# Optimization experiments

Hardware: AMD Instinct MI355X
Metric: run time of the kernel (lower is better)

The kernel has to match this reference:

```python
import jax, jax.numpy as jnp
import numpy as np

B, S, D = 1, 2048, 4096
H, HK, HD = 32, 8, 128  # query heads, kv heads, head dim
T_CACHE = 2048
N_REP = H // HK


def setup_inputs() -> dict:
    key = jax.random.key(0)
    ks = jax.random.split(key, 8)
    x = jax.random.normal(ks[0], (B, S, D), dtype=jnp.float32)
    # multiplicative rope factor, broadcast over head axis
    rope = jax.random.uniform(ks[1], (1, S, 1, HD), dtype=jnp.float32, minval=-1.0, maxval=1.0)
    cache_k = jax.random.normal(ks[2], (B, T_CACHE, HK, HD), dtype=jnp.float32)
    cache_v = jax.random.normal(ks[3], (B, T_CACHE, HK, HD), dtype=jnp.float32)
    wq = jax.random.normal(ks[4], (D, H * HD), dtype=jnp.float32) * 0.02
    wk = jax.random.normal(ks[5], (D, HK * HD), dtype=jnp.float32) * 0.02
    wv = jax.random.normal(ks[6], (D, HK * HD), dtype=jnp.float32) * 0.02
    wo = jax.random.normal(ks[7], (H * HD, D), dtype=jnp.float32) * 0.02
    # mask: [1, 1, S, T_CACHE + S]; attend freely to cache, causal within new chunk
    neg = np.float32(-1e9)
    causal = np.triu(np.full((S, S), neg, dtype=np.float32), k=1)
    mask = np.concatenate([np.zeros((S, T_CACHE), dtype=np.float32), causal], axis=1)
    mask = jnp.asarray(mask)[None, None, :, :]
    return {"x": x, "rope": rope, "mask": mask, "cache_k": cache_k,
            "cache_v": cache_v, "wq": wq, "wk": wk, "wv": wv, "wo": wo}


def reference(x, rope, mask, cache_k, cache_v, wq, wk, wv, wo):
    b, s, _ = x.shape
    scale = 1.0 / np.sqrt(HD).astype(np.float32)
    xq = (x @ wq).reshape(b, s, H, HD) * rope          # [b, s, H, hd]
    xk = (x @ wk).reshape(b, s, HK, HD) * rope         # [b, s, HK, hd]
    xv = (x @ wv).reshape(b, s, HK, HD)
    keys = jnp.concatenate([cache_k, xk], axis=1)      # [b, t, HK, hd]
    vals = jnp.concatenate([cache_v, xv], axis=1)
    keys = jnp.repeat(keys, N_REP, axis=2)             # GQA repeat -> [b, t, H, hd]
    vals = jnp.repeat(vals, N_REP, axis=2)
    scores = jnp.einsum('bshd,bthd->bhst', xq, keys) * scale
    scores = scores + mask
    probs = jax.nn.softmax(scores.astype(jnp.float32), axis=-1).astype(xq.dtype)
    out = jnp.einsum('bhst,bthd->bshd', probs, vals).reshape(b, s, H * HD)
    return out @ wo
```

## Files before the change

### kernel.cpp

```cpp
#include <hip/hip_runtime.h>

typedef unsigned short u16;
typedef unsigned int   u32;
typedef short  s16x8 __attribute__((ext_vector_type(8)));
typedef float  f32x4 __attribute__((ext_vector_type(4)));

__device__ __forceinline__ u16 f2bf(float f) {
    union { float f; u32 i; } x; x.f = f;
    u32 r = x.i + 0x7FFFu + ((x.i >> 16) & 1u);
    return (u16)(r >> 16);
}

__device__ __forceinline__ void gld16(const void* g, void* l) {
    __builtin_amdgcn_global_load_lds((const __attribute__((address_space(1))) void*)g,
                                     (__attribute__((address_space(3))) void*)l,
                                     16, 0, 0);
}

__global__ __launch_bounds__(256)
void cast_bf16(const float* __restrict__ in, u16* __restrict__ out, int n4) {
    int g = blockIdx.x * 256 + threadIdx.x;
    if (g >= n4) return;
    float4 v = ((const float4*)in)[g];
    ushort4 o; o.x = f2bf(v.x); o.y = f2bf(v.y); o.z = f2bf(v.z); o.w = f2bf(v.w);
    ((ushort4*)out)[g] = o;
}

__global__ __launch_bounds__(256)
void tconv(const float* __restrict__ B, u16* __restrict__ Bt, int K, int N) {
    __shared__ float T[32][33];
    int n0 = blockIdx.x * 32, k0 = blockIdx.y * 32;
    int t = threadIdx.x;
    int r = t >> 3, c4 = (t & 7) * 4;
    float4 v = *(const float4*)&B[(size_t)(k0 + r) * N + n0 + c4];
    T[r][c4 + 0] = v.x; T[r][c4 + 1] = v.y; T[r][c4 + 2] = v.z; T[r][c4 + 3] = v.w;
    __syncthreads();
    ushort4 o;
    o.x = f2bf(T[c4 + 0][r]); o.y = f2bf(T[c4 + 1][r]);
    o.z = f2bf(T[c4 + 2][r]); o.w = f2bf(T[c4 + 3][r]);
    *(ushort4*)&Bt[(size_t)(n0 + r) * K + k0 + c4] = o;
}

__global__ __launch_bounds__(256)
void kcache_conv(const float* __restrict__ ck, u16* __restrict__ Kc) {
    int g = blockIdx.x * 256 + threadIdx.x;
    int d = (g & 31) * 4, kh = (g >> 5) & 7, t = g >> 8;
    float4 v = *(const float4*)&ck[(size_t)t * 1024 + kh * 128 + d];
    ushort4 o; o.x = f2bf(v.x); o.y = f2bf(v.y); o.z = f2bf(v.z); o.w = f2bf(v.w);
    *(ushort4*)&Kc[(size_t)kh * 524288 + (size_t)t * 128 + d] = o;
}

__global__ __launch_bounds__(256)
void vcache_conv(const float* __restrict__ cv, u16* __restrict__ Vt) {
    __shared__ float T[32][33];
    int t0 = blockIdx.x * 32, d0 = blockIdx.y * 32, kh = blockIdx.z;
    int t = threadIdx.x;
    int r = t >> 3, c4 = (t & 7) * 4;
    float4 v = *(const float4*)&cv[(size_t)(t0 + r) * 1024 + kh * 128 + d0 + c4];
    T[r][c4 + 0] = v.x; T[r][c4 + 1] = v.y; T[r][c4 + 2] = v.z; T[r][c4 + 3] = v.w;
    __syncthreads();
    ushort4 o;
    o.x = f2bf(T[c4 + 0][r]); o.y = f2bf(T[c4 + 1][r]);
    o.z = f2bf(T[c4 + 2][r]); o.w = f2bf(T[c4 + 3][r]);
    *(ushort4*)&Vt[(size_t)(kh * 128 + d0 + r) * 4096 + t0 + c4] = o;
}

__device__ __forceinline__ void gemm_core(const u16* __restrict__ A,
                                          const u16* __restrict__ Bt,
                                          int K, int m0,
                                          u16* As, u16* Bs, f32x4 acc[4][4])
{
    const int tid = threadIdx.x;
    const int lane = tid & 63, w = tid >> 6;
    const int quad = lane >> 4, l15 = lane & 15;
    const int mw = (w >> 1) * 64, nw = (w & 1) * 64;
    const int lrow = tid >> 2;
    const int lcol = ((tid & 3) ^ (lrow & 3)) * 8;
    const int rsw = l15 & 3;

    for (int k0 = 0; k0 < K; k0 += 32) {
        __syncthreads();
        gld16(A  + (size_t)(m0 +      lrow) * K + k0 + lcol, &As[w * 512]);
        gld16(A  + (size_t)(m0 + 64 + lrow) * K + k0 + lcol, &As[2048 + w * 512]);
        gld16(Bt + (size_t)(           lrow) * K + k0 + lcol, &Bs[w * 512]);
        gld16(Bt + (size_t)(      64 + lrow) * K + k0 + lcol, &Bs[2048 + w * 512]);
        __syncthreads();
        s16x8 af[4], bf[4];
        #pragma unroll
        for (int i = 0; i < 4; ++i)
            af[i] = *(const s16x8*)&As[(mw + i * 16 + l15) * 32 + (quad ^ rsw) * 8];
        #pragma unroll
        for (int j = 0; j < 4; ++j)
            bf[j] = *(const s16x8*)&Bs[(nw + j * 16 + l15) * 32 + (quad ^ rsw) * 8];
        #pragma unroll
        for (int i = 0; i < 4; ++i)
            #pragma unroll
            for (int j = 0; j < 4; ++j)
                acc[i][j] = __builtin_amdgcn_mfma_f32_16x16x32_bf16(
                    af[i], bf[j], acc[i][j], 0, 0, 0);
    }
}

__global__ __launch_bounds__(256, 2)
void gemm_qkv(const u16* __restrict__ A, const u16* __restrict__ Wq,
              const u16* __restrict__ Wk, const u16* __restrict__ Wv,
              u16* __restrict__ Qw, u16* __restrict__ Kc, u16* __restrict__ Vt,
              const float* __restrict__ rope)
{
    __shared__ u16 As[128 * 32];
    __shared__ u16 Bs[128 * 32];
    const int m0 = blockIdx.y * 128, n0 = blockIdx.x * 128;

    const u16* Bt;
    if (n0 < 4096)       Bt = Wq + (size_t)n0 * 4096;
    else if (n0 < 5120)  Bt = Wk + (size_t)(n0 - 4096) * 4096;
    else                 Bt = Wv + (size_t)(n0 - 5120) * 4096;

    f32x4 acc[4][4];
    #pragma unroll
    for (int i = 0; i < 4; ++i)
        #pragma unroll
        for (int j = 0; j < 4; ++j) acc[i][j] = (f32x4)0.f;

    gemm_core(A, Bt, 4096, m0, As, Bs, acc);

    const int lane = threadIdx.x & 63, w = threadIdx.x >> 6;
    const int quad = lane >> 4, l15 = lane & 15;
    const int mw = (w >> 1) * 64, nw = (w & 1) * 64;

    #pragma unroll
    for (int i = 0; i < 4; ++i) {
        #pragma unroll
        for (int j = 0; j < 4; ++j) {
            int mm = m0 + mw + i * 16 + quad * 4;
            int nn = n0 + nw + j * 16 + l15;
            if (nn < 4096) {
                #pragma unroll
                for (int r = 0; r < 4; ++r)
                    Qw[(size_t)(mm + r) * 4096 + nn] =
                        f2bf(acc[i][j][r] * rope[(size_t)(mm + r) * 128 + (nn & 127)]
                             * 0.08838834764831845f);
            } else if (nn < 5120) {
                #pragma unroll
                for (int r = 0; r < 4; ++r)
                    Kc[(size_t)((nn - 4096) >> 7) * 524288
                       + (size_t)(2048 + mm + r) * 128 + (nn & 127)] =
                        f2bf(acc[i][j][r] * rope[(size_t)(mm + r) * 128 + (nn & 127)]);
            } else {
                ushort4 o;
                o.x = f2bf(acc[i][j][0]); o.y = f2bf(acc[i][j][1]);
                o.z = f2bf(acc[i][j][2]); o.w = f2bf(acc[i][j][3]);
                *(ushort4*)&Vt[(size_t)(nn - 5120) * 4096 + 2048 + mm] = o;
            }
        }
    }
}

__global__ __launch_bounds__(256, 2)
void gemm_wo(const u16* __restrict__ A, const u16* __restrict__ Bt,
             float* __restrict__ C)
{
    __shared__ u16 As[128 * 32];
    __shared__ u16 Bs[128 * 32];
    const int m0 = blockIdx.y * 128, n0 = blockIdx.x * 128;

    f32x4 acc[4][4];
    #pragma unroll
    for (int i = 0; i < 4; ++i)
        #pragma unroll
        for (int j = 0; j < 4; ++j) acc[i][j] = (f32x4)0.f;

    gemm_core(A, Bt + (size_t)n0 * 4096, 4096, m0, As, Bs, acc);

    const int lane = threadIdx.x & 63, w = threadIdx.x >> 6;
    const int quad = lane >> 4, l15 = lane & 15;
    const int mw = (w >> 1) * 64, nw = (w & 1) * 64;

    #pragma unroll
    for (int i = 0; i < 4; ++i)
        #pragma unroll
        for (int j = 0; j < 4; ++j) {
            int mm = m0 + mw + i * 16 + quad * 4;
            int nn = n0 + nw + j * 16 + l15;
            #pragma unroll
            for (int r = 0; r < 4; ++r)
                C[(size_t)(mm + r) * 4096 + nn] = acc[i][j][r];
        }
}

__global__ __launch_bounds__(256, 4)
void attn_mfma(const u16* __restrict__ Qw, const u16* __restrict__ Kc,
               const u16* __restrict__ Vt, u16* __restrict__ AO)
{
    __shared__ u16 KsBuf[2][32 * 128];
    __shared__ u16 VsBuf[2][128 * 32];
    __shared__ u16 PbBuf[2][64 * 32];

    const int tid = threadIdx.x;
    const int lane = tid & 63, w = tid >> 6;
    const int quad = lane >> 4, l15 = lane & 15;

    const int bid = blockIdx.x + 32 * blockIdx.y;
    const int kh = bid & 7;
    const int inner = bid >> 3;
    const int h = kh * 4 + (inner & 3);
    const int q0 = (inner >> 2) * 64;

    const int kw = w & 1, qw = w >> 1;
    const size_t kvb = (size_t)kh * 524288;

    s16x8 qreg[2][4];
    #pragma unroll
    for (int n = 0; n < 2; ++n)
        #pragma unroll
        for (int ks = 0; ks < 4; ++ks)
            qreg[n][ks] = *(const s16x8*)&Qw[(size_t)(q0 + qw * 32 + n * 16 + l15) * 4096
                                             + h * 128 + ks * 32 + quad * 8];

    f32x4 o[2][4];
    #pragma unroll
    for (int m = 0; m < 2; ++m)
        #pragma unroll
        for (int n = 0; n < 4; ++n) o[m][n] = (f32x4)0.f;
    float lacc[2] = {0.f, 0.f};

    const int krow = tid >> 4, kcol = ((tid & 15) ^ (krow & 15)) * 8;
    const int vrow = tid >> 2, vcol = ((tid & 3) ^ ((vrow >> 1) & 3)) * 8;

    const u16* kpg = Kc + kvb + (size_t)krow * 128 + kcol;
    const u16* vpg = Vt + kvb + (size_t)vrow * 4096 + vcol;

    const int kend = 2112 + q0;

    u16* ks_rd = &KsBuf[0][0]; u16* ks_st = &KsBuf[1][0];
    u16* vs_rd = &VsBuf[1][0]; u16* vs_st = &VsBuf[0][0];
    u16* pb_wr = &PbBuf[0][0]; u16* pb_rd = &PbBuf[1][0];

    auto PV = [&](const u16* vs, const u16* pb) {
        int vr0 = w * 32 + l15;
        int vr1 = w * 32 + 16 + l15;
        s16x8 vf0 = *(const s16x8*)&vs[vr0 * 32 + (quad ^ ((vr0 >> 1) & 3)) * 8];
        s16x8 vf1 = *(const s16x8*)&vs[vr1 * 32 + (quad ^ ((vr1 >> 1) & 3)) * 8];
        #pragma unroll
        for (int n = 0; n < 4; ++n) {
            int q = n * 16 + l15;
            s16x8 pf = *(const s16x8*)&pb[q * 32 + ((quad ^ (q & 3)) * 8)];
            o[0][n] = __builtin_amdgcn_mfma_f32_16x16x32_bf16(vf0, pf, o[0][n], 0, 0, 0);
            o[1][n] = __builtin_amdgcn_mfma_f32_16x16x32_bf16(vf1, pf, o[1][n], 0, 0, 0);
        }
    };

    gld16(kpg,        &ks_rd[w * 512]);
    gld16(kpg + 2048, &ks_rd[2048 + w * 512]);

    for (int t0 = 0; t0 < kend; t0 += 32) {
        __syncthreads();

        if (t0 + 32 < kend) {
            gld16(kpg + (size_t)(t0 + 32) * 128,        &ks_st[w * 512]);
            gld16(kpg + (size_t)(t0 + 32) * 128 + 2048, &ks_st[2048 + w * 512]);
        }
        gld16(vpg + t0,          &vs_st[w * 512]);
        gld16(vpg + 262144 + t0, &vs_st[2048 + w * 512]);

        f32x4 sc[2];
        sc[0] = (f32x4)0.f; sc[1] = (f32x4)0.f;
        #pragma unroll
        for (int ks = 0; ks < 4; ++ks) {
            int kc8 = (((ks * 4 + quad) ^ l15) & 15) * 8;
            s16x8 kf = *(const s16x8*)&ks_rd[(kw * 16 + l15) * 128 + kc8];
            sc[0] = __builtin_amdgcn_mfma_f32_16x16x32_bf16(kf, qreg[0][ks], sc[0], 0, 0, 0);
            sc[1] = __builtin_amdgcn_mfma_f32_16x16x32_bf16(kf, qreg[1][ks], sc[1], 0, 0, 0);
        }

        const bool maskt = (t0 + 31 > 2048 + q0);
        #pragma unroll
        for (int n2 = 0; n2 < 2; ++n2) {
            float e0 = __expf(sc[n2][0]);
            float e1 = __expf(sc[n2][1]);
            float e2 = __expf(sc[n2][2]);
            float e3 = __expf(sc[n2][3]);
            if (maskt) {
                int key = t0 + kw * 16 + quad * 4;
                int qv  = q0 + qw * 32 + n2 * 16 + l15;
                if (key + 0 >= 2048 && key + 0 - 2048 > qv) e0 = 0.f;
                if (key + 1 >= 2048 && key + 1 - 2048 > qv) e1 = 0.f;
                if (key + 2 >= 2048 && key + 2 - 2048 > qv) e2 = 0.f;
                if (key + 3 >= 2048 && key + 3 - 2048 > qv) e3 = 0.f;
            }
            lacc[n2] += (e0 + e1) + (e2 + e3);
            u32 p0, p1;
            asm("v_cvt_pk_bf16_f32 %0, %1, %2" : "=v"(p0) : "v"(e0), "v"(e1));
            asm("v_cvt_pk_bf16_f32 %0, %1, %2" : "=v"(p1) : "v"(e2), "v"(e3));
            int q = qw * 32 + n2 * 16 + l15;
            uint2 pk; pk.x = p0; pk.y = p1;
            *(uint2*)&pb_wr[q * 32 + (((2 * kw + (quad >> 1)) ^ (q & 3)) * 8)
                            + (quad & 1) * 4] = pk;
        }

        if (t0) PV(vs_rd, pb_rd);

        u16* tp;
        tp = ks_rd; ks_rd = ks_st; ks_st = tp;
        tp = vs_rd; vs_rd = vs_st; vs_st = tp;
        tp = pb_rd; pb_rd = pb_wr; pb_wr = tp;
    }

    __syncthreads();
    PV(vs_rd, pb_rd);

    float* Ls = (float*)&KsBuf[0][0];
    lacc[0] += __shfl_xor(lacc[0], 16); lacc[0] += __shfl_xor(lacc[0], 32);
    lacc[1] += __shfl_xor(lacc[1], 16); lacc[1] += __shfl_xor(lacc[1], 32);
    if (lane < 16) {
        Ls[kw * 64 + qw * 32 +      lane] = lacc[0];
        Ls[kw * 64 + qw * 32 + 16 + lane] = lacc[1];
    }
    __syncthreads();

    #pragma unroll
    for (int n = 0; n < 4; ++n) {
        int qq = n * 16 + l15;
        float inv = 1.f / (Ls[qq] + Ls[64 + qq]);
        #pragma unroll
        for (int m = 0; m < 2; ++m) {
            ushort4 ov;
            ov.x = f2bf(o[m][n][0] * inv);
            ov.y = f2bf(o[m][n][1] * inv);
            ov.z = f2bf(o[m][n][2] * inv);
            ov.w = f2bf(o[m][n][3] * inv);
            *(ushort4*)&AO[(size_t)(q0 + qq) * 4096 + h * 128
                           + w * 32 + m * 16 + quad * 4] = ov;
        }
    }
}

extern "C" void kernel_launch(void* const* d_in, const int* in_sizes, int n_in,
                              void* d_out, int out_size, void* d_ws, size_t ws_size,
                              hipStream_t stream)
{
    const float* x      = (const float*)d_in[0];
    const float* rope   = (const float*)d_in[1];
    const float* cacheK = (const float*)d_in[3];
    const float* cacheV = (const float*)d_in[4];
    const float* wq     = (const float*)d_in[5];
    const float* wk     = (const float*)d_in[6];
    const float* wv     = (const float*)d_in[7];
    const float* wo     = (const float*)d_in[8];
    float* out = (float*)d_out;

    u16* xb = (u16*)d_ws;
    u16* W0 = xb + (size_t)8388608;
    u16* W1 = W0 + (size_t)16777216;
    u16* Qw = W1 + (size_t)4194304;
    u16* Kc = Qw + (size_t)8388608;
    u16* Vt = Kc + (size_t)4194304;
    u16* AO = Vt + (size_t)4194304;
    u16* Wv = AO;

    dim3 blk(256);
    cast_bf16<<<dim3(8192), blk, 0, stream>>>(x, xb, 2097152);
    tconv<<<dim3(128, 128), blk, 0, stream>>>(wq, W0, 4096, 4096);
    tconv<<<dim3(32, 128), blk, 0, stream>>>(wk, W1, 4096, 1024);
    tconv<<<dim3(32, 128), blk, 0, stream>>>(wv, Wv, 4096, 1024);
    gemm_qkv<<<dim3(48, 16), blk, 0, stream>>>(xb, W0, W1, Wv, Qw, Kc, Vt, rope);
    kcache_conv<<<dim3(2048), blk, 0, stream>>>(cacheK, Kc);
    vcache_conv<<<dim3(64, 4, 8), blk, 0, stream>>>(cacheV, Vt);
    attn_mfma<<<dim3(32, 32), blk, 0, stream>>>(Qw, Kc, Vt, AO);
    tconv<<<dim3(128, 128), blk, 0, stream>>>(wo, W0, 4096, 4096);
    gemm_wo<<<dim3(32, 16), blk, 0, stream>>>(AO, W0, out);
}
```

Measured before the change: 592.9 us.

## Load K and V fragments straight to registers, dropping LDS staging in attention

The attention kernel stops staging K and V tiles through shared memory with async global-to-LDS copies. Each wave now loads its MFMA fragments directly from global memory into registers, double-buffering K fragments across a two-step unrolled loop. The P buffer becomes padded (stride 40) instead of XOR-swizzled, and occupancy bounds drop from 4 to 3 blocks per SM. This removes LDS traffic and bank-conflict handling, but adds redundant global loads across waves that share K rows and raises register pressure.

```diff
diff --git a/kernel.cpp b/kernel.cpp
--- a/kernel.cpp
+++ b/kernel.cpp
@@ -188,13 +188,11 @@
         }
 }
 
-__global__ __launch_bounds__(256, 4)
+__global__ __launch_bounds__(256, 3)
 void attn_mfma(const u16* __restrict__ Qw, const u16* __restrict__ Kc,
                const u16* __restrict__ Vt, u16* __restrict__ AO)
 {
-    __shared__ u16 KsBuf[2][32 * 128];
-    __shared__ u16 VsBuf[2][128 * 32];
-    __shared__ u16 PbBuf[2][64 * 32];
+    __shared__ u16 PbBuf[2][64 * 40];
 
     const int tid = threadIdx.x;
     const int lane = tid & 63, w = tid >> 6;
@@ -224,94 +222,102 @@
         for (int n = 0; n < 4; ++n) o[m][n] = (f32x4)0.f;
     float lacc[2] = {0.f, 0.f};
 
-    const int krow = tid >> 4, kcol = ((tid & 15) ^ (krow & 15)) * 8;
-    const int vrow = tid >> 2, vcol = ((tid & 3) ^ ((vrow >> 1) & 3)) * 8;
-
-    const u16* kpg = Kc + kvb + (size_t)krow * 128 + kcol;
-    const u16* vpg = Vt + kvb + (size_t)vrow * 4096 + vcol;
+    const u16* kfp  = Kc + kvb + (size_t)(kw * 16 + l15) * 128 + quad * 8;
+    const u16* vfp0 = Vt + kvb + (size_t)(w * 32 + l15) * 4096 + quad * 8;
+    const u16* vfp1 = vfp0 + (size_t)16 * 4096;
 
     const int kend = 2112 + q0;
 
-    u16* ks_rd = &KsBuf[0][0]; u16* ks_st = &KsBuf[1][0];
-    u16* vs_rd = &VsBuf[1][0]; u16* vs_st = &VsBuf[0][0];
-    u16* pb_wr = &PbBuf[0][0]; u16* pb_rd = &PbBuf[1][0];
-
-    auto PV = [&](const u16* vs, const u16* pb) {
-        int vr0 = w * 32 + l15;
-        int vr1 = w * 32 + 16 + l15;
-        s16x8 vf0 = *(const s16x8*)&vs[vr0 * 32 + (quad ^ ((vr0 >> 1) & 3)) * 8];
-        s16x8 vf1 = *(const s16x8*)&vs[vr1 * 32 + (quad ^ ((vr1 >> 1) & 3)) * 8];
+    u16* pb_wr = &PbBuf[0][0];
+    u16* pb_rd = &PbBuf[1][0];
+
+    s16x8 kA0, kA1, kA2, kA3, kB0, kB1, kB2, kB3;
+    kA0 = *(const s16x8*)&kfp[0];
+    kA1 = *(const s16x8*)&kfp[32];
+    kA2 = *(const s16x8*)&kfp[64];
+    kA3 = *(const s16x8*)&kfp[96];
+
+#define AITER(T0, C0, C1, C2, C3, N0, N1, N2, N3)                              \
+    {                                                                          \
+        const int tt = (T0);                                                   \
+           \
+        __syncthreads();                                                       \
+            \
+        s16x8 vf0 = *(const s16x8*)&vfp0[tt - 32];                             \
+        s16x8 vf1 = *(const s16x8*)&vfp1[tt - 32];                             \
+                        \
+        { const u16* knp = kfp + (size_t)(tt + 32) * 128;                      \
+          N0 = *(const s16x8*)&knp[0];                                         \
+          N1 = *(const s16x8*)&knp[32];                                        \
+          N2 = *(const s16x8*)&knp[64];                                        \
+          N3 = *(const s16x8*)&knp[96]; }                                      \
+                    \
+        f32x4 sc0 = (f32x4)0.f, sc1 = (f32x4)0.f;                              \
+        sc0 = __builtin_amdgcn_mfma_f32_16x16x32_bf16(C0, qreg[0][0], sc0, 0, 0, 0); \
+        sc1 = __builtin_amdgcn_mfma_f32_16x16x32_bf16(C0, qreg[1][0], sc1, 0, 0, 0); \
+        sc0 = __builtin_amdgcn_mfma_f32_16x16x32_bf16(C1, qreg[0][1], sc0, 0, 0, 0); \
+        sc1 = __builtin_amdgcn_mfma_f32_16x16x32_bf16(C1, qreg[1][1], sc1, 0, 0, 0); \
+        sc0 = __builtin_amdgcn_mfma_f32_16x16x32_bf16(C2, qreg[0][2], sc0, 0, 0, 0); \
+        sc1 = __builtin_amdgcn_mfma_f32_16x16x32_bf16(C2, qreg[1][2], sc1, 0, 0, 0); \
+        sc0 = __builtin_amdgcn_mfma_f32_16x16x32_bf16(C3, qreg[0][3], sc0, 0, 0, 0); \
+        sc1 = __builtin_amdgcn_mfma_f32_16x16x32_bf16(C3, qreg[1][3], sc1, 0, 0, 0); \
+        const bool maskt = (tt + 31 > 2048 + q0);                              \
+        _Pragma("unroll")                                                      \
+        for (int n2 = 0; n2 < 2; ++n2) {                                       \
+            f32x4 s = n2 ? sc1 : sc0;                                          \
+            float e0 = __expf(s[0]);                                           \
+            float e1 = __expf(s[1]);                                           \
+            float e2 = __expf(s[2]);                                           \
+            float e3 = __expf(s[3]);                                           \
+            if (maskt) {                                                       \
+                int key = tt + kw * 16 + quad * 4;                             \
+                int qv  = q0 + qw * 32 + n2 * 16 + l15;                        \
+                if (key + 0 >= 2048 && key + 0 - 2048 > qv) e0 = 0.f;          \
+                if (key + 1 >= 2048 && key + 1 - 2048 > qv) e1 = 0.f;          \
+                if (key + 2 >= 2048 && key + 2 - 2048 > qv) e2 = 0.f;          \
+                if (key + 3 >= 2048 && key + 3 - 2048 > qv) e3 = 0.f;          \
+            }                                                                  \
+            lacc[n2] += (e0 + e1) + (e2 + e3);                                 \
+            u32 p0, p1;                                                        \
+            asm("v_cvt_pk_bf16_f32 %0, %1, %2" : "=v"(p0) : "v"(e0), "v"(e1)); \
+            asm("v_cvt_pk_bf16_f32 %0, %1, %2" : "=v"(p1) : "v"(e2), "v"(e3)); \
+            uint2 pk; pk.x = p0; pk.y = p1;                                    \
+            *(uint2*)&pb_wr[(qw * 32 + n2 * 16 + l15) * 40 + kw * 16 + quad * 4] = pk; \
+        }                                                                      \
+                    \
+        if (tt) {                                                              \
+            _Pragma("unroll")                                                  \
+            for (int n = 0; n < 4; ++n) {                                      \
+                s16x8 pf = *(const s16x8*)&pb_rd[(n * 16 + l15) * 40 + quad * 8]; \
+                o[0][n] = __builtin_amdgcn_mfma_f32_16x16x32_bf16(vf0, pf, o[0][n], 0, 0, 0); \
+                o[1][n] = __builtin_amdgcn_mfma_f32_16x16x32_bf16(vf1, pf, o[1][n], 0, 0, 0); \
+            }                                                                  \
+        }                                                                      \
+        { u16* tp = pb_rd; pb_rd = pb_wr; pb_wr = tp; }                        \
+    }
+
+    for (int t0 = 0; t0 < kend; t0 += 64) {
+        AITER(t0,      kA0, kA1, kA2, kA3, kB0, kB1, kB2, kB3)
+        AITER(t0 + 32, kB0, kB1, kB2, kB3, kA0, kA1, kA2, kA3)
+    }
+#undef AITER
+
+    __syncthreads();
+    {
+        s16x8 vf0 = *(const s16x8*)&vfp0[kend - 32];
+        s16x8 vf1 = *(const s16x8*)&vfp1[kend - 32];
         #pragma unroll
         for (int n = 0; n < 4; ++n) {
-            int q = n * 16 + l15;
-            s16x8 pf = *(const s16x8*)&pb[q * 32 + ((quad ^ (q & 3)) * 8)];
+            s16x8 pf = *(const s16x8*)&pb_rd[(n * 16 + l15) * 40 + quad * 8];
             o[0][n] = __builtin_amdgcn_mfma_f32_16x16x32_bf16(vf0, pf, o[0][n], 0, 0, 0);
             o[1][n] = __builtin_amdgcn_mfma_f32_16x16x32_bf16(vf1, pf, o[1][n], 0, 0, 0);
         }
-    };
-
-    gld16(kpg,        &ks_rd[w * 512]);
-    gld16(kpg + 2048, &ks_rd[2048 + w * 512]);
-
-    for (int t0 = 0; t0 < kend; t0 += 32) {
-        __syncthreads();
-
-        if (t0 + 32 < kend) {
-            gld16(kpg + (size_t)(t0 + 32) * 128,        &ks_st[w * 512]);
-            gld16(kpg + (size_t)(t0 + 32) * 128 + 2048, &ks_st[2048 + w * 512]);
-        }
-        gld16(vpg + t0,          &vs_st[w * 512]);
-        gld16(vpg + 262144 + t0, &vs_st[2048 + w * 512]);
-
-        f32x4 sc[2];
-        sc[0] = (f32x4)0.f; sc[1] = (f32x4)0.f;
-        #pragma unroll
-        for (int ks = 0; ks < 4; ++ks) {
-            int kc8 = (((ks * 4 + quad) ^ l15) & 15) * 8;
-            s16x8 kf = *(const s16x8*)&ks_rd[(kw * 16 + l15) * 128 + kc8];
-            sc[0] = __builtin_amdgcn_mfma_f32_16x16x32_bf16(kf, qreg[0][ks], sc[0], 0, 0, 0);
-            sc[1] = __builtin_amdgcn_mfma_f32_16x16x32_bf16(kf, qreg[1][ks], sc[1], 0, 0, 0);
-        }
-
-        const bool maskt = (t0 + 31 > 2048 + q0);
-        #pragma unroll
-        for (int n2 = 0; n2 < 2; ++n2) {
-            float e0 = __expf(sc[n2][0]);
-            float e1 = __expf(sc[n2][1]);
-            float e2 = __expf(sc[n2][2]);
-            float e3 = __expf(sc[n2][3]);
-            if (maskt) {
-                int key = t0 + kw * 16 + quad * 4;
-                int qv  = q0 + qw * 32 + n2 * 16 + l15;
-                if (key + 0 >= 2048 && key + 0 - 2048 > qv) e0 = 0.f;
-                if (key + 1 >= 2048 && key + 1 - 2048 > qv) e1 = 0.f;
-                if (key + 2 >= 2048 && key + 2 - 2048 > qv) e2 = 0.f;
-                if (key + 3 >= 2048 && key + 3 - 2048 > qv) e3 = 0.f;
-            }
-            lacc[n2] += (e0 + e1) + (e2 + e3);
-            u32 p0, p1;
-            asm("v_cvt_pk_bf16_f32 %0, %1, %2" : "=v"(p0) : "v"(e0), "v"(e1));
-            asm("v_cvt_pk_bf16_f32 %0, %1, %2" : "=v"(p1) : "v"(e2), "v"(e3));
-            int q = qw * 32 + n2 * 16 + l15;
-            uint2 pk; pk.x = p0; pk.y = p1;
-            *(uint2*)&pb_wr[q * 32 + (((2 * kw + (quad >> 1)) ^ (q & 3)) * 8)
-                            + (quad & 1) * 4] = pk;
-        }
-
-        if (t0) PV(vs_rd, pb_rd);
-
-        u16* tp;
-        tp = ks_rd; ks_rd = ks_st; ks_st = tp;
-        tp = vs_rd; vs_rd = vs_st; vs_st = tp;
-        tp = pb_rd; pb_rd = pb_wr; pb_wr = tp;
-    }
-
-    __syncthreads();
-    PV(vs_rd, pb_rd);
-
-    float* Ls = (float*)&KsBuf[0][0];
+    }
+
+    float* Ls = (float*)&PbBuf[0][0];
     lacc[0] += __shfl_xor(lacc[0], 16); lacc[0] += __shfl_xor(lacc[0], 32);
     lacc[1] += __shfl_xor(lacc[1], 16); lacc[1] += __shfl_xor(lacc[1], 32);
+    __syncthreads();
     if (lane < 16) {
         Ls[kw * 64 + qw * 32 +      lane] = lacc[0];
         Ls[kw * 64 + qw * 32 + 16 + lane] = lacc[1];
```

After: 725.8 us. 22.4% more time.
